# Optimization experiments

Hardware: AMD Instinct MI355X
Metric: run time of the kernel (lower is better)

Reference implementation:

```python
import jax, jax.numpy as jnp
import numpy as np

BN_EPS = 1e-5


def setup_inputs() -> dict:
    key = jax.random.key(0)
    ks = jax.random.split(key, 14)
    B, N, C, NS = 2, 1024, 512, 64
    seed_xyz = jax.random.uniform(ks[0], (B, N, 3), jnp.float32)          # points in unit cube
    seed_features = jax.random.normal(ks[1], (B, C, N), jnp.float32)
    # per-seed rotation matrices (orthonormalized via QR)
    rot = jnp.linalg.qr(jax.random.normal(ks[2], (B, N, 3, 3), jnp.float32))[0]
    # cuboid extents sized so each query finds a reasonable neighbor count
    crop_size = 0.2 + 0.3 * jax.random.uniform(ks[3], (B, N, 3), jnp.float32)
    W1 = jax.random.normal(ks[4], (256, 3 + C), jnp.float32) / np.float32(np.sqrt(3 + C))
    gamma1 = 1.0 + 0.1 * jax.random.normal(ks[5], (256,), jnp.float32)
    beta1 = 0.1 * jax.random.normal(ks[6], (256,), jnp.float32)
    mean1 = 0.1 * jax.random.normal(ks[7], (256,), jnp.float32)
    var1 = 0.5 + jax.random.uniform(ks[8], (256,), jnp.float32)
    W2 = jax.random.normal(ks[9], (256, 256), jnp.float32) / np.float32(16.0)
    gamma2 = 1.0 + 0.1 * jax.random.normal(ks[10], (256,), jnp.float32)
    beta2 = 0.1 * jax.random.normal(ks[11], (256,), jnp.float32)
    mean2 = 0.1 * jax.random.normal(ks[12], (256,), jnp.float32)
    var2 = 0.5 + jax.random.uniform(ks[13], (256,), jnp.float32)
    return dict(seed_xyz=seed_xyz, seed_features=seed_features, rot=rot,
                crop_size=crop_size, W1=W1, gamma1=gamma1, beta1=beta1,
                mean1=mean1, var1=var1, W2=W2, gamma2=gamma2, beta2=beta2,
                mean2=mean2, var2=var2, nsample=NS)


def _conv_bn_relu(x, W, g, b, m, v):
    # 1x1 conv (no bias, bn=True) + inference BatchNorm + ReLU
    y = jnp.einsum('bpnc,oc->bpno', x, W)
    scale = g * jax.lax.rsqrt(v + BN_EPS)
    return jax.nn.relu((y - m) * scale + b)


def reference(seed_xyz, seed_features, rot, crop_size,
              W1, gamma1, beta1, mean1, var1,
              W2, gamma2, beta2, mean2, var2, nsample):
    # ---- rotated rectangular query + group (queries == points == seed_xyz) ----
    # diff[b,p,n] = xyz[b,n] - query[b,p]; rotate into the query's local frame
    diff = seed_xyz[:, None, :, :] - seed_xyz[:, :, None, :]          # (B,P,N,3)
    local = jnp.einsum('bpnj,bpjk->bpnk', diff, rot)                  # (B,P,N,3)
    inside = jnp.all(jnp.abs(local) <= 0.5 * crop_size[:, :, None, :], axis=-1)  # (B,P,N)
    # first `nsample` in-region indices, invalid slots filled with the first hit
    order = jnp.argsort(jnp.where(inside, 0, 1).astype(jnp.int32), axis=-1, stable=True)
    idx = order[..., :nsample]                                        # (B,P,NS)
    valid = jnp.take_along_axis(inside, idx, axis=-1)
    idx = jnp.where(valid, idx, idx[..., :1])
    # gather rotated local xyz and features
    g_xyz = jnp.take_along_axis(local, idx[..., None], axis=2)        # (B,P,NS,3)
    feats = jnp.swapaxes(seed_features, 1, 2)                         # (B,N,C)
    g_feat = jax.vmap(lambda f, i: f[i])(feats, idx)                  # (B,P,NS,C)
    grouped = jnp.concatenate([g_xyz, g_feat], axis=-1)               # (B,P,NS,3+C)
    # ---- SharedMLP (1x1 conv + BN + ReLU) x2, then max over samples ----
    h = _conv_bn_relu(grouped, W1, gamma1, beta1, mean1, var1)
    h = _conv_bn_relu(h, W2, gamma2, beta2, mean2, var2)
    out = jnp.max(h, axis=2)                                          # (B,P,256)
    return jnp.swapaxes(out, 1, 2)                                    # (B,256,P)
```

## Files before the change

kernel.cpp:

```cpp
#include <hip/hip_runtime.h>
#include <hip/hip_bf16.h>
#include <math.h>

typedef __attribute__((ext_vector_type(8))) __bf16 bf16x8;
typedef __attribute__((ext_vector_type(4))) __bf16 bf16x4;
typedef __attribute__((ext_vector_type(2))) __bf16 bf16x2;
typedef __attribute__((ext_vector_type(4))) float f32x4;

#define NPTS 1024
#define CIN 512
#define NSAMP 64
#define LDFT 520
#define LDFO 136

__device__ __forceinline__ void local_coords(const float* q, float cx, float cy, float cz,
                                             const float R[9], float& l0, float& l1, float& l2) {
    float d0 = __fsub_rn(q[0], cx);
    float d1 = __fsub_rn(q[1], cy);
    float d2 = __fsub_rn(q[2], cz);
    l0 = __fadd_rn(__fadd_rn(__fmul_rn(d0, R[0]), __fmul_rn(d1, R[3])), __fmul_rn(d2, R[6]));
    l1 = __fadd_rn(__fadd_rn(__fmul_rn(d0, R[1]), __fmul_rn(d1, R[4])), __fmul_rn(d2, R[7]));
    l2 = __fadd_rn(__fadd_rn(__fmul_rn(d0, R[2]), __fmul_rn(d1, R[5])), __fmul_rn(d2, R[8]));
}

__global__ __launch_bounds__(256) void setup_kernel(
    const float* __restrict__ xyz, const float* __restrict__ rot,
    const float* __restrict__ crop,
    const float* __restrict__ W1, const float* __restrict__ W2,
    const float* __restrict__ g1, const float* __restrict__ be1,
    const float* __restrict__ m1, const float* __restrict__ v1,
    const float* __restrict__ g2, const float* __restrict__ be2,
    const float* __restrict__ m2, const float* __restrict__ v2,
    __bf16* __restrict__ W1f, __bf16* __restrict__ W2s,
    float* __restrict__ wxs,
    float* __restrict__ s1, float* __restrict__ b1,
    float* __restrict__ s2, float* __restrict__ b2,
    unsigned short* __restrict__ seln_g, int* __restrict__ cnt_g,
    f32x4* __restrict__ lcsel_g) {
    __shared__ __align__(16) f32x4 lcall[NPTS];
    __shared__ unsigned long long msk[16];
    __shared__ int wpre[17];
    __shared__ int selr[NSAMP];

    const int t = threadIdx.x;
    if (blockIdx.x < 256) {
        const int o = blockIdx.x;
        if (t == 0) {
            float sc1 = g1[o] / sqrtf(v1[o] + 1e-5f);
            s1[o] = sc1;
            b1[o] = be1[o] - m1[o] * sc1;
            float sc2 = g2[o] / sqrtf(v2[o] + 1e-5f);
            s2[o] = sc2;
            b2[o] = be2[o] - m2[o] * sc2;
            wxs[o * 4 + 0] = sc1 * W1[o * 515 + 0];
            wxs[o * 4 + 1] = sc1 * W1[o * 515 + 1];
            wxs[o * 4 + 2] = sc1 * W1[o * 515 + 2];
            wxs[o * 4 + 3] = 0.f;
        }
        for (int k = t; k < CIN; k += blockDim.x)
            W1f[o * CIN + k] = (__bf16)W1[o * 515 + 3 + k];
        {
            const int f = o * 256 + t;
            const int j = f & 7;
            const int l = (f >> 3) & 63;
            const int nt = (f >> 9) & 1;
            const int ks = (f >> 10) & 7;
            const int w = (f >> 13) & 7;
            const int o2 = w * 32 + nt * 16 + (l & 15);
            const int k = ks * 32 + ((l >> 4) << 3) + j;
            W2s[f] = (__bf16)W2[o2 * 256 + k];
        }
        return;
    }
    const int bid = blockIdx.x - 256;
    const int b = bid >> 10;
    const int l = t & 63, w = t >> 6;

    const float cx = xyz[bid * 3 + 0], cy = xyz[bid * 3 + 1], cz = xyz[bid * 3 + 2];
    float R[9];
#pragma unroll
    for (int j = 0; j < 9; ++j) R[j] = rot[bid * 9 + j];
    const float h0 = 0.5f * crop[bid * 3 + 0];
    const float h1 = 0.5f * crop[bid * 3 + 1];
    const float h2 = 0.5f * crop[bid * 3 + 2];

#pragma unroll
    for (int i = 0; i < 4; ++i) {
        const int n = i * 256 + t;
        float l0, l1, l2;
        local_coords(xyz + (size_t)(b * NPTS + n) * 3, cx, cy, cz, R, l0, l1, l2);
        lcall[n] = f32x4{l0, l1, l2, 0.f};
        bool ins = (__builtin_fabsf(l0) <= h0) && (__builtin_fabsf(l1) <= h1) &&
                   (__builtin_fabsf(l2) <= h2);
        unsigned long long bal = __ballot(ins);
        if (l == 0) msk[i * 4 + w] = bal;
    }
    __syncthreads();
    if (t < 64) {
        const int c = (t < 16) ? __popcll(msk[t]) : 0;
        int sum = c;
#pragma unroll
        for (int d = 1; d < 16; d <<= 1) {
            int v = __shfl_up(sum, d);
            if (t >= d) sum += v;
        }
        if (t < 16) wpre[t] = sum - c;
        if (t == 15) wpre[16] = sum;
    }
    __syncthreads();
    const int cnt = wpre[16];
#pragma unroll
    for (int i = 0; i < 4; ++i) {
        const int n = i * 256 + t;
        const unsigned long long wd = msk[n >> 6];
        const int bit = n & 63;
        if ((wd >> bit) & 1ull) {
            int rank = wpre[n >> 6] + __popcll(wd & ((1ull << bit) - 1ull));
            if (rank < NSAMP) selr[rank] = n;
        }
    }
    __syncthreads();
    if (t < NSAMP) {
        const int n = selr[(t < cnt) ? t : 0];
        seln_g[(size_t)bid * NSAMP + t] = (unsigned short)n;
        lcsel_g[(size_t)bid * NSAMP + t] = lcall[n];
    }
    if (t == 0) cnt_g[bid] = cnt;
}

__global__ __launch_bounds__(256) void fgemm_kernel(const float* __restrict__ feats,
                                                    const __bf16* __restrict__ W1f,
                                                    const float* __restrict__ s1,
                                                    const float* __restrict__ b1,
                                                    __bf16* __restrict__ Fsb) {
    __shared__ __align__(16) __bf16 Ft[16][LDFT];
    __shared__ __align__(16) __bf16 Fo[16][LDFO];
    const int t = threadIdx.x;
    const int b = blockIdx.x >> 7;
    const int half = (blockIdx.x >> 6) & 1;
    const int n0 = (blockIdx.x & 63) << 4;
    const int l = t & 63, w = t >> 6;
    const int lo = l & 15, kg = l >> 4;

    const float* fb = feats + (size_t)b * (CIN * NPTS) + n0;
    {
        const int n = t & 15;
        const int cq = (t >> 4) * 2;
        for (int i = 0; i < 16; ++i) {
            int c = i * 32 + cq;
            float v0 = fb[(size_t)c * NPTS + n];
            float v1v = fb[(size_t)(c + 1) * NPTS + n];
            bf16x2 pk = {(__bf16)v0, (__bf16)v1v};
            *(bf16x2*)(&Ft[n][c]) = pk;
        }
    }
    __syncthreads();

    f32x4 acc[2];
#pragma unroll
    for (int mt = 0; mt < 2; ++mt) acc[mt] = f32x4{0.f, 0.f, 0.f, 0.f};

#pragma unroll
    for (int ks = 0; ks < 16; ++ks) {
        const int kk = ks * 32 + kg * 8;
        const bf16x8 bfr = *(const bf16x8*)(&Ft[lo][kk]);
#pragma unroll
        for (int mt = 0; mt < 2; ++mt) {
            const int o = half * 128 + w * 32 + mt * 16 + lo;
            const bf16x8 af = *(const bf16x8*)(&W1f[(size_t)o * CIN + kk]);
            acc[mt] = __builtin_amdgcn_mfma_f32_16x16x32_bf16(af, bfr, acc[mt], 0, 0, 0);
        }
    }
    __syncthreads();
#pragma unroll
    for (int mt = 0; mt < 2; ++mt) {
        const int ol = w * 32 + mt * 16 + kg * 4;
        const f32x4 sv = *(const f32x4*)(&s1[half * 128 + ol]);
        const f32x4 bv = *(const f32x4*)(&b1[half * 128 + ol]);
        bf16x4 r;
#pragma unroll
        for (int j = 0; j < 4; ++j) r[j] = (__bf16)fmaf(acc[mt][j], sv[j], bv[j]);
        *(bf16x4*)(&Fo[lo][ol]) = r;
    }
    __syncthreads();
    {
        const int row = t >> 4, c = t & 15;
        const bf16x8 v = *(const bf16x8*)(&Fo[row][c * 8]);
        *(bf16x8*)(&Fsb[((size_t)(b * NPTS + n0 + row)) * 256 + half * 128 + c * 8]) = v;
    }
}

__global__ __launch_bounds__(512, 2) void fused_kernel(
    const __bf16* __restrict__ Fsb, const float* __restrict__ wxs,
    const unsigned short* __restrict__ seln_g, const int* __restrict__ cnt_g,
    const f32x4* __restrict__ lcsel_g,
    const __bf16* __restrict__ W2s, const float* __restrict__ s2g, const float* __restrict__ b2g,
    float* __restrict__ out) {
    __shared__ __align__(16) char A2raw[NSAMP * 512];
    __shared__ __align__(16) f32x4 lcL[4][NSAMP];
    __shared__ __align__(16) float outst[256][4];
    __shared__ unsigned short selL[4][NSAMP];
    __shared__ int cntL[4];

    const int raw = (int)blockIdx.x;
    const int pg = (raw & 7) * 64 + (raw >> 3);
    const int b = pg >> 8;
    const int p0 = (pg & 255) * 4;
    const int t = threadIdx.x;
    const int l = t & 63, w = t >> 6;
    const int lo = l & 15, kg = l >> 4;

    if (t < 256) {
        const int pi = t >> 6, s = t & 63;
        const size_t base = ((size_t)(b * NPTS + p0 + pi)) * NSAMP + s;
        selL[pi][s] = seln_g[base];
        lcL[pi][s] = lcsel_g[base];
    }
    if (t >= 256 && t < 260) cntL[t - 256] = cnt_g[b * NPTS + p0 + (t - 256)];

    bf16x8 wf[8][2];
#pragma unroll
    for (int ks = 0; ks < 8; ++ks)
#pragma unroll
        for (int nt = 0; nt < 2; ++nt)
            wf[ks][nt] = *(const bf16x8*)(&W2s[(size_t)((((w * 8 + ks) * 2 + nt) * 64) + l) * 8]);

    const int oc = (t & 31) * 8;
    const int sg = t >> 5;
    f32x4 wv[8];
#pragma unroll
    for (int j = 0; j < 8; ++j) wv[j] = *(const f32x4*)(&wxs[(oc + j) * 4]);

    float sc[2], bb[2];
#pragma unroll
    for (int nt = 0; nt < 2; ++nt) {
        const int o = w * 32 + nt * 16 + lo;
        sc[nt] = s2g[o];
        bb[nt] = b2g[o];
    }
    __syncthreads();

    bf16x8 stg[4];
    {
        const int rpad = (min(cntL[0], NSAMP) + 15) & ~15;
#pragma unroll
        for (int si = 0; si < 4; ++si) {
            const int s = sg * 4 + si;
            if (s < rpad) {
                const int n = (int)selL[0][s];
                stg[si] = *(const bf16x8*)(&Fsb[((size_t)(b * NPTS + n)) * 256 + oc]);
            }
        }
#pragma unroll
        for (int si = 0; si < 4; ++si) {
            const int s = sg * 4 + si;
            if (s < rpad) {
                const f32x4 cd = lcL[0][s];
                bf16x8 pk;
#pragma unroll
                for (int j = 0; j < 8; ++j) {
                    const float x = fmaf(cd.x, wv[j].x,
                                         fmaf(cd.y, wv[j].y,
                                              fmaf(cd.z, wv[j].z, (float)stg[si][j])));
                    pk[j] = (__bf16)fmaxf(x, 0.f);
                }
                *(bf16x8*)(A2raw + s * 512 + ((oc * 2) ^ ((s & 7) << 4))) = pk;
            }
        }
    }
    __syncthreads();

    for (int pi = 0; pi < 4; ++pi) {
        const int mtmax = (min(cntL[pi], NSAMP) + 15) >> 4;

        int rpadn = 0;
        if (pi < 3) {
            rpadn = (min(cntL[pi + 1], NSAMP) + 15) & ~15;
#pragma unroll
            for (int si = 0; si < 4; ++si) {
                const int s = sg * 4 + si;
                if (s < rpadn) {
                    const int n = (int)selL[pi + 1][s];
                    stg[si] = *(const bf16x8*)(&Fsb[((size_t)(b * NPTS + n)) * 256 + oc]);
                }
            }
        }

        f32x4 acc[4][2];
#pragma unroll
        for (int mt = 0; mt < 4; ++mt)
#pragma unroll
            for (int nt = 0; nt < 2; ++nt)
                acc[mt][nt] = f32x4{0.f, 0.f, 0.f, 0.f};

#pragma unroll
        for (int mt = 0; mt < 4; ++mt) {
            if (mt < mtmax) {
                const int row = mt * 16 + lo;
#pragma unroll
                for (int ks = 0; ks < 8; ++ks) {
                    const bf16x8 a = *(const bf16x8*)(A2raw + row * 512 +
                                                      ((ks * 64 + kg * 16) ^ ((row & 7) << 4)));
                    acc[mt][0] = __builtin_amdgcn_mfma_f32_16x16x32_bf16(a, wf[ks][0],
                                                                         acc[mt][0], 0, 0, 0);
                    acc[mt][1] = __builtin_amdgcn_mfma_f32_16x16x32_bf16(a, wf[ks][1],
                                                                         acc[mt][1], 0, 0, 0);
                }
            }
        }

#pragma unroll
        for (int nt = 0; nt < 2; ++nt) {
            float mx = 0.f;
#pragma unroll
            for (int mt = 0; mt < 4; ++mt) {
                if (mt < mtmax) {
#pragma unroll
                    for (int r = 0; r < 4; ++r)
                        mx = fmaxf(mx, fmaxf(fmaf(acc[mt][nt][r], sc[nt], bb[nt]), 0.f));
                }
            }
            mx = fmaxf(mx, __shfl_xor(mx, 16));
            mx = fmaxf(mx, __shfl_xor(mx, 32));
            if (kg == 0) outst[w * 32 + nt * 16 + lo][pi] = mx;
        }
        __syncthreads();

        if (pi < 3) {
#pragma unroll
            for (int si = 0; si < 4; ++si) {
                const int s = sg * 4 + si;
                if (s < rpadn) {
                    const f32x4 cd = lcL[pi + 1][s];
                    bf16x8 pk;
#pragma unroll
                    for (int j = 0; j < 8; ++j) {
                        const float x = fmaf(cd.x, wv[j].x,
                                             fmaf(cd.y, wv[j].y,
                                                  fmaf(cd.z, wv[j].z, (float)stg[si][j])));
                        pk[j] = (__bf16)fmaxf(x, 0.f);
                    }
                    *(bf16x8*)(A2raw + s * 512 + ((oc * 2) ^ ((s & 7) << 4))) = pk;
                }
            }
        }
        __syncthreads();
    }

    if (t < 256) {
        const int o = t;
        const f32x4 v = *(const f32x4*)(&outst[o][0]);
        *(f32x4*)(&out[((size_t)b * 256 + o) * NPTS + p0]) = v;
    }
}

extern "C" void kernel_launch(void* const* d_in, const int* in_sizes, int n_in,
                              void* d_out, int out_size, void* d_ws, size_t ws_size,
                              hipStream_t stream) {
    (void)in_sizes; (void)n_in; (void)out_size; (void)ws_size;
    const float* xyz   = (const float*)d_in[0];
    const float* feats = (const float*)d_in[1];
    const float* rot   = (const float*)d_in[2];
    const float* crop  = (const float*)d_in[3];
    const float* W1    = (const float*)d_in[4];
    const float* g1    = (const float*)d_in[5];
    const float* be1   = (const float*)d_in[6];
    const float* m1    = (const float*)d_in[7];
    const float* v1    = (const float*)d_in[8];
    const float* W2    = (const float*)d_in[9];
    const float* g2    = (const float*)d_in[10];
    const float* be2   = (const float*)d_in[11];
    const float* m2    = (const float*)d_in[12];
    const float* v2    = (const float*)d_in[13];

    char* ws = (char*)d_ws;
    __bf16* W1f = (__bf16*)(ws + 0);
    __bf16* W2s = (__bf16*)(ws + 262144);
    float*  wxs = (float*)(ws + 393216);
    float*  s1  = (float*)(ws + 397312);
    float*  b1  = (float*)(ws + 398336);
    float*  s2  = (float*)(ws + 399360);
    float*  b2  = (float*)(ws + 400384);
    __bf16* Fsb = (__bf16*)(ws + 401408);
    unsigned short* seln = (unsigned short*)(ws + 1449984);
    int*    cntg = (int*)(ws + 1712128);
    f32x4*  lcse = (f32x4*)(ws + 1720320);

    setup_kernel<<<2304, 256, 0, stream>>>(xyz, rot, crop,
                                           W1, W2, g1, be1, m1, v1, g2, be2, m2, v2,
                                           W1f, W2s, wxs, s1, b1, s2, b2, seln, cntg, lcse);
    fgemm_kernel<<<256, 256, 0, stream>>>(feats, W1f, s1, b1, Fsb);
    fused_kernel<<<512, 512, 0, stream>>>(Fsb, wxs, seln, cntg, lcse, W2s, s2, b2,
                                          (float*)d_out);
}
```

Baseline: 46.53 us.

## Merge feature GEMM into setup kernel and restructure fused-kernel gather staging

Folds the feature×W1 GEMM into the setup kernel as extra blocks. It reads W1 fp32 directly with an inline bf16 conversion instead of going through a pre-converted W1f buffer, which removes one kernel launch and its dependency on setup. The fused kernel now gives each thread 4 channels × 8 samples instead of 8 × 4, moves the xyz-term FMA and ReLU to before the max-reduction barrier, and raises launch_bounds occupancy from 2 to 4. Costs: W1 is reread and converted per block, and register pressure is tighter at the higher occupancy.

```diff
diff --git a/kernel.cpp b/kernel.cpp
--- a/kernel.cpp
+++ b/kernel.cpp
@@ -25,30 +25,92 @@
 
 __global__ __launch_bounds__(256) void setup_kernel(
     const float* __restrict__ xyz, const float* __restrict__ rot,
-    const float* __restrict__ crop,
+    const float* __restrict__ crop, const float* __restrict__ feats,
     const float* __restrict__ W1, const float* __restrict__ W2,
     const float* __restrict__ g1, const float* __restrict__ be1,
     const float* __restrict__ m1, const float* __restrict__ v1,
     const float* __restrict__ g2, const float* __restrict__ be2,
     const float* __restrict__ m2, const float* __restrict__ v2,
-    __bf16* __restrict__ W1f, __bf16* __restrict__ W2s,
-    float* __restrict__ wxs,
-    float* __restrict__ s1, float* __restrict__ b1,
+    __bf16* __restrict__ W2s, float* __restrict__ wxs,
     float* __restrict__ s2, float* __restrict__ b2,
+    __bf16* __restrict__ Fsb,
     unsigned short* __restrict__ seln_g, int* __restrict__ cnt_g,
     f32x4* __restrict__ lcsel_g) {
-    __shared__ __align__(16) f32x4 lcall[NPTS];
-    __shared__ unsigned long long msk[16];
-    __shared__ int wpre[17];
-    __shared__ int selr[NSAMP];
-
+    __shared__ __align__(16) char U[22016];
     const int t = threadIdx.x;
+
     if (blockIdx.x < 256) {
-        const int o = blockIdx.x;
+        __bf16(*Ft)[LDFT] = (__bf16(*)[LDFT])(U);
+        __bf16(*Fo)[LDFO] = (__bf16(*)[LDFO])(U + 16640);
+        float* s1l = (float*)(U + 20992);
+        float* b1l = (float*)(U + 21504);
+        const int rb = blockIdx.x;
+        const int b = rb >> 7, half = (rb >> 6) & 1, n0 = (rb & 63) << 4;
+        const int l = t & 63, w = t >> 6;
+        const int lo = l & 15, kg = l >> 4;
+
+        if (t < 128) {
+            const int o = half * 128 + t;
+            const float s = g1[o] / sqrtf(v1[o] + 1e-5f);
+            s1l[t] = s;
+            b1l[t] = be1[o] - m1[o] * s;
+        }
+        const float* fb = feats + (size_t)b * (CIN * NPTS) + n0;
+        {
+            const int n = t & 15;
+            const int cq = (t >> 4) * 2;
+            for (int i = 0; i < 16; ++i) {
+                int c = i * 32 + cq;
+                float v0 = fb[(size_t)c * NPTS + n];
+                float v1v = fb[(size_t)(c + 1) * NPTS + n];
+                bf16x2 pk = {(__bf16)v0, (__bf16)v1v};
+                *(bf16x2*)(&Ft[n][c]) = pk;
+            }
+        }
+        __syncthreads();
+
+        f32x4 acc[2];
+#pragma unroll
+        for (int mt = 0; mt < 2; ++mt) acc[mt] = f32x4{0.f, 0.f, 0.f, 0.f};
+
+#pragma unroll
+        for (int ks = 0; ks < 16; ++ks) {
+            const int kk = ks * 32 + kg * 8;
+            const bf16x8 bfr = *(const bf16x8*)(&Ft[lo][kk]);
+#pragma unroll
+            for (int mt = 0; mt < 2; ++mt) {
+                const int o = half * 128 + w * 32 + mt * 16 + lo;
+                const float* wrow = W1 + (size_t)o * 515 + 3 + kk;
+                bf16x8 af;
+#pragma unroll
+                for (int j = 0; j < 8; ++j) af[j] = (__bf16)wrow[j];
+                acc[mt] = __builtin_amdgcn_mfma_f32_16x16x32_bf16(af, bfr, acc[mt], 0, 0, 0);
+            }
+        }
+        __syncthreads();
+#pragma unroll
+        for (int mt = 0; mt < 2; ++mt) {
+            const int ol = w * 32 + mt * 16 + kg * 4;
+            const f32x4 sv = *(const f32x4*)(&s1l[ol]);
+            const f32x4 bv = *(const f32x4*)(&b1l[ol]);
+            bf16x4 r;
+#pragma unroll
+            for (int j = 0; j < 4; ++j) r[j] = (__bf16)fmaf(acc[mt][j], sv[j], bv[j]);
+            *(bf16x4*)(&Fo[lo][ol]) = r;
+        }
+        __syncthreads();
+        {
+            const int row = t >> 4, c = t & 15;
+            const bf16x8 v = *(const bf16x8*)(&Fo[row][c * 8]);
+            *(bf16x8*)(&Fsb[((size_t)(b * NPTS + n0 + row)) * 256 + half * 128 + c * 8]) = v;
+        }
+        return;
+    }
+
+    if (blockIdx.x < 512) {
+        const int o = blockIdx.x - 256;
         if (t == 0) {
             float sc1 = g1[o] / sqrtf(v1[o] + 1e-5f);
-            s1[o] = sc1;
-            b1[o] = be1[o] - m1[o] * sc1;
             float sc2 = g2[o] / sqrtf(v2[o] + 1e-5f);
             s2[o] = sc2;
             b2[o] = be2[o] - m2[o] * sc2;
@@ -57,8 +119,6 @@
             wxs[o * 4 + 2] = sc1 * W1[o * 515 + 2];
             wxs[o * 4 + 3] = 0.f;
         }
-        for (int k = t; k < CIN; k += blockDim.x)
-            W1f[o * CIN + k] = (__bf16)W1[o * 515 + 3 + k];
         {
             const int f = o * 256 + t;
             const int j = f & 7;
@@ -72,7 +132,12 @@
         }
         return;
     }
-    const int bid = blockIdx.x - 256;
+
+    f32x4* lcall = (f32x4*)(U);
+    unsigned long long* msk = (unsigned long long*)(U + 16384);
+    int* wpre = (int*)(U + 16512);
+    int* selr = (int*)(U + 16584);
+    const int bid = blockIdx.x - 512;
     const int b = bid >> 10;
     const int l = t & 63, w = t >> 6;
 
@@ -128,69 +193,7 @@
     if (t == 0) cnt_g[bid] = cnt;
 }
 
-__global__ __launch_bounds__(256) void fgemm_kernel(const float* __restrict__ feats,
-                                                    const __bf16* __restrict__ W1f,
-                                                    const float* __restrict__ s1,
-                                                    const float* __restrict__ b1,
-                                                    __bf16* __restrict__ Fsb) {
-    __shared__ __align__(16) __bf16 Ft[16][LDFT];
-    __shared__ __align__(16) __bf16 Fo[16][LDFO];
-    const int t = threadIdx.x;
-    const int b = blockIdx.x >> 7;
-    const int half = (blockIdx.x >> 6) & 1;
-    const int n0 = (blockIdx.x & 63) << 4;
-    const int l = t & 63, w = t >> 6;
-    const int lo = l & 15, kg = l >> 4;
-
-    const float* fb = feats + (size_t)b * (CIN * NPTS) + n0;
-    {
-        const int n = t & 15;
-        const int cq = (t >> 4) * 2;
-        for (int i = 0; i < 16; ++i) {
-            int c = i * 32 + cq;
-            float v0 = fb[(size_t)c * NPTS + n];
-            float v1v = fb[(size_t)(c + 1) * NPTS + n];
-            bf16x2 pk = {(__bf16)v0, (__bf16)v1v};
-            *(bf16x2*)(&Ft[n][c]) = pk;
-        }
-    }
-    __syncthreads();
-
-    f32x4 acc[2];
-#pragma unroll
-    for (int mt = 0; mt < 2; ++mt) acc[mt] = f32x4{0.f, 0.f, 0.f, 0.f};
-
-#pragma unroll
-    for (int ks = 0; ks < 16; ++ks) {
-        const int kk = ks * 32 + kg * 8;
-        const bf16x8 bfr = *(const bf16x8*)(&Ft[lo][kk]);
-#pragma unroll
-        for (int mt = 0; mt < 2; ++mt) {
-            const int o = half * 128 + w * 32 + mt * 16 + lo;
-            const bf16x8 af = *(const bf16x8*)(&W1f[(size_t)o * CIN + kk]);
-            acc[mt] = __builtin_amdgcn_mfma_f32_16x16x32_bf16(af, bfr, acc[mt], 0, 0, 0);
-        }
-    }
-    __syncthreads();
-#pragma unroll
-    for (int mt = 0; mt < 2; ++mt) {
-        const int ol = w * 32 + mt * 16 + kg * 4;
-        const f32x4 sv = *(const f32x4*)(&s1[half * 128 + ol]);
-        const f32x4 bv = *(const f32x4*)(&b1[half * 128 + ol]);
-        bf16x4 r;
-#pragma unroll
-        for (int j = 0; j < 4; ++j) r[j] = (__bf16)fmaf(acc[mt][j], sv[j], bv[j]);
-        *(bf16x4*)(&Fo[lo][ol]) = r;
-    }
-    __syncthreads();
-    {
-        const int row = t >> 4, c = t & 15;
-        const bf16x8 v = *(const bf16x8*)(&Fo[row][c * 8]);
-        *(bf16x8*)(&Fsb[((size_t)(b * NPTS + n0 + row)) * 256 + half * 128 + c * 8]) = v;
-    }
-}
-
-__global__ __launch_bounds__(512, 2) void fused_kernel(
+__global__ __launch_bounds__(512, 4) void fused_kernel(
     const __bf16* __restrict__ Fsb, const float* __restrict__ wxs,
     const unsigned short* __restrict__ seln_g, const int* __restrict__ cnt_g,
     const f32x4* __restrict__ lcsel_g,
@@ -225,11 +228,11 @@
         for (int nt = 0; nt < 2; ++nt)
             wf[ks][nt] = *(const bf16x8*)(&W2s[(size_t)((((w * 8 + ks) * 2 + nt) * 64) + l) * 8]);
 
-    const int oc = (t & 31) * 8;
-    const int sg = t >> 5;
-    f32x4 wv[8];
-#pragma unroll
-    for (int j = 0; j < 8; ++j) wv[j] = *(const f32x4*)(&wxs[(oc + j) * 4]);
+    const int oc4 = (t & 63) * 4;
+    const int g8 = t >> 6;
+    f32x4 wv4[4];
+#pragma unroll
+    for (int j = 0; j < 4; ++j) wv4[j] = *(const f32x4*)(&wxs[(oc4 + j) * 4]);
 
     float sc[2], bb[2];
 #pragma unroll
@@ -240,31 +243,30 @@
     }
     __syncthreads();
 
-    bf16x8 stg[4];
+    bf16x4 stg[8];
     {
         const int rpad = (min(cntL[0], NSAMP) + 15) & ~15;
 #pragma unroll
-        for (int si = 0; si < 4; ++si) {
-            const int s = sg * 4 + si;
+        for (int si = 0; si < 8; ++si) {
+            const int s = g8 * 8 + si;
             if (s < rpad) {
                 const int n = (int)selL[0][s];
-                stg[si] = *(const bf16x8*)(&Fsb[((size_t)(b * NPTS + n)) * 256 + oc]);
-            }
-        }
-#pragma unroll
-        for (int si = 0; si < 4; ++si) {
-            const int s = sg * 4 + si;
+                stg[si] = *(const bf16x4*)(&Fsb[((size_t)(b * NPTS + n)) * 256 + oc4]);
+            }
+        }
+#pragma unroll
+        for (int si = 0; si < 8; ++si) {
+            const int s = g8 * 8 + si;
             if (s < rpad) {
                 const f32x4 cd = lcL[0][s];
-                bf16x8 pk;
-#pragma unroll
-                for (int j = 0; j < 8; ++j) {
-                    const float x = fmaf(cd.x, wv[j].x,
-                                         fmaf(cd.y, wv[j].y,
-                                              fmaf(cd.z, wv[j].z, (float)stg[si][j])));
-                    pk[j] = (__bf16)fmaxf(x, 0.f);
-                }
-                *(bf16x8*)(A2raw + s * 512 + ((oc * 2) ^ ((s & 7) << 4))) = pk;
+#pragma unroll
+                for (int j = 0; j < 4; ++j) {
+                    const float x = fmaf(cd.x, wv4[j].x,
+                                         fmaf(cd.y, wv4[j].y,
+                                              fmaf(cd.z, wv4[j].z, (float)stg[si][j])));
+                    stg[si][j] = (__bf16)fmaxf(x, 0.f);
+                }
+                *(bf16x4*)(A2raw + s * 512 + ((oc4 * 2) ^ ((s & 7) << 4))) = stg[si];
             }
         }
     }
@@ -272,16 +274,15 @@
 
     for (int pi = 0; pi < 4; ++pi) {
         const int mtmax = (min(cntL[pi], NSAMP) + 15) >> 4;
-
         int rpadn = 0;
         if (pi < 3) {
             rpadn = (min(cntL[pi + 1], NSAMP) + 15) & ~15;
 #pragma unroll
-            for (int si = 0; si < 4; ++si) {
-                const int s = sg * 4 + si;
+            for (int si = 0; si < 8; ++si) {
+                const int s = g8 * 8 + si;
                 if (s < rpadn) {
                     const int n = (int)selL[pi + 1][s];
-                    stg[si] = *(const bf16x8*)(&Fsb[((size_t)(b * NPTS + n)) * 256 + oc]);
+                    stg[si] = *(const bf16x4*)(&Fsb[((size_t)(b * NPTS + n)) * 256 + oc4]);
                 }
             }
         }
@@ -309,6 +310,23 @@
             }
         }
 
+        if (pi < 3) {
+#pragma unroll
+            for (int si = 0; si < 8; ++si) {
+                const int s = g8 * 8 + si;
+                if (s < rpadn) {
+                    const f32x4 cd = lcL[pi + 1][s];
+#pragma unroll
+                    for (int j = 0; j < 4; ++j) {
+                        const float x = fmaf(cd.x, wv4[j].x,
+                                             fmaf(cd.y, wv4[j].y,
+                                                  fmaf(cd.z, wv4[j].z, (float)stg[si][j])));
+                        stg[si][j] = (__bf16)fmaxf(x, 0.f);
+                    }
+                }
+            }
+        }
+
 #pragma unroll
         for (int nt = 0; nt < 2; ++nt) {
             float mx = 0.f;
@@ -328,20 +346,10 @@
 
         if (pi < 3) {
 #pragma unroll
-            for (int si = 0; si < 4; ++si) {
-                const int s = sg * 4 + si;
-                if (s < rpadn) {
-                    const f32x4 cd = lcL[pi + 1][s];
-                    bf16x8 pk;
-#pragma unroll
-                    for (int j = 0; j < 8; ++j) {
-                        const float x = fmaf(cd.x, wv[j].x,
-                                             fmaf(cd.y, wv[j].y,
-                                                  fmaf(cd.z, wv[j].z, (float)stg[si][j])));
-                        pk[j] = (__bf16)fmaxf(x, 0.f);
-                    }
-                    *(bf16x8*)(A2raw + s * 512 + ((oc * 2) ^ ((s & 7) << 4))) = pk;
-                }
+            for (int si = 0; si < 8; ++si) {
+                const int s = g8 * 8 + si;
+                if (s < rpadn)
+                    *(bf16x4*)(A2raw + s * 512 + ((oc4 * 2) ^ ((s & 7) << 4))) = stg[si];
             }
         }
         __syncthreads();
@@ -374,22 +382,18 @@
     const float* v2    = (const float*)d_in[13];
 
     char* ws = (char*)d_ws;
-    __bf16* W1f = (__bf16*)(ws + 0);
-    __bf16* W2s = (__bf16*)(ws + 262144);
-    float*  wxs = (float*)(ws + 393216);
-    float*  s1  = (float*)(ws + 397312);
-    float*  b1  = (float*)(ws + 398336);
-    float*  s2  = (float*)(ws + 399360);
-    float*  b2  = (float*)(ws + 400384);
-    __bf16* Fsb = (__bf16*)(ws + 401408);
-    unsigned short* seln = (unsigned short*)(ws + 1449984);
-    int*    cntg = (int*)(ws + 1712128);
-    f32x4*  lcse = (f32x4*)(ws + 1720320);
-
-    setup_kernel<<<2304, 256, 0, stream>>>(xyz, rot, crop,
+    __bf16* W2s = (__bf16*)(ws + 0);
+    float*  wxs = (float*)(ws + 131072);
+    float*  s2  = (float*)(ws + 135168);
+    float*  b2  = (float*)(ws + 136192);
+    __bf16* Fsb = (__bf16*)(ws + 137216);
+    unsigned short* seln = (unsigned short*)(ws + 1185792);
+    int*    cntg = (int*)(ws + 1447936);
+    f32x4*  lcse = (f32x4*)(ws + 1456128);
+
+    setup_kernel<<<2560, 256, 0, stream>>>(xyz, rot, crop, feats,
                                            W1, W2, g1, be1, m1, v1, g2, be2, m2, v2,
-                                           W1f, W2s, wxs, s1, b1, s2, b2, seln, cntg, lcse);
-    fgemm_kernel<<<256, 256, 0, stream>>>(feats, W1f, s1, b1, Fsb);
+                                           W2s, wxs, s2, b2, Fsb, seln, cntg, lcse);
     fused_kernel<<<512, 512, 0, stream>>>(Fsb, wxs, seln, cntg, lcse, W2s, s2, b2,
                                           (float*)d_out);
 }
```

After: 110.7 us. 2.38x slower.

## Process eight query points per block and overlap layer-1 epilogue with MFMA

Applied to the files above, without the earlier changes.

Each fused-kernel block now handles eight query points instead of four, so half as many blocks are launched and the W2 register fragments are loaded once per eight points. The gather split changes from eight channels per thread to four channels over eight samples. The per-sample xyz correction and ReLU for the next point is now computed in registers right after the MFMA loop and before the barrier, leaving only the shared-memory store after it. In exchange, 256 blocks fill fewer CUs and each block runs a longer serial chain.

```diff
diff --git a/kernel.cpp b/kernel.cpp
--- a/kernel.cpp
+++ b/kernel.cpp
@@ -197,26 +197,26 @@
     const __bf16* __restrict__ W2s, const float* __restrict__ s2g, const float* __restrict__ b2g,
     float* __restrict__ out) {
     __shared__ __align__(16) char A2raw[NSAMP * 512];
-    __shared__ __align__(16) f32x4 lcL[4][NSAMP];
-    __shared__ __align__(16) float outst[256][4];
-    __shared__ unsigned short selL[4][NSAMP];
-    __shared__ int cntL[4];
+    __shared__ __align__(16) f32x4 lcL[8][NSAMP];
+    __shared__ __align__(16) float outst[256][8];
+    __shared__ unsigned short selL[8][NSAMP];
+    __shared__ int cntL[8];
 
     const int raw = (int)blockIdx.x;
-    const int pg = (raw & 7) * 64 + (raw >> 3);
-    const int b = pg >> 8;
-    const int p0 = (pg & 255) * 4;
+    const int pg = (raw & 7) * 32 + (raw >> 3);
+    const int b = pg >> 7;
+    const int p0 = (pg & 127) * 8;
     const int t = threadIdx.x;
     const int l = t & 63, w = t >> 6;
     const int lo = l & 15, kg = l >> 4;
 
-    if (t < 256) {
+    {
         const int pi = t >> 6, s = t & 63;
         const size_t base = ((size_t)(b * NPTS + p0 + pi)) * NSAMP + s;
         selL[pi][s] = seln_g[base];
         lcL[pi][s] = lcsel_g[base];
     }
-    if (t >= 256 && t < 260) cntL[t - 256] = cnt_g[b * NPTS + p0 + (t - 256)];
+    if (t < 8) cntL[t] = cnt_g[b * NPTS + p0 + t];
 
     bf16x8 wf[8][2];
 #pragma unroll
@@ -225,11 +225,11 @@
         for (int nt = 0; nt < 2; ++nt)
             wf[ks][nt] = *(const bf16x8*)(&W2s[(size_t)((((w * 8 + ks) * 2 + nt) * 64) + l) * 8]);
 
-    const int oc = (t & 31) * 8;
-    const int sg = t >> 5;
-    f32x4 wv[8];
-#pragma unroll
-    for (int j = 0; j < 8; ++j) wv[j] = *(const f32x4*)(&wxs[(oc + j) * 4]);
+    const int oc4 = (t & 63) * 4;
+    const int g8 = t >> 6;
+    f32x4 wv4[4];
+#pragma unroll
+    for (int j = 0; j < 4; ++j) wv4[j] = *(const f32x4*)(&wxs[(oc4 + j) * 4]);
 
     float sc[2], bb[2];
 #pragma unroll
@@ -240,48 +240,46 @@
     }
     __syncthreads();
 
-    bf16x8 stg[4];
+    bf16x4 stg[8];
     {
         const int rpad = (min(cntL[0], NSAMP) + 15) & ~15;
 #pragma unroll
-        for (int si = 0; si < 4; ++si) {
-            const int s = sg * 4 + si;
+        for (int si = 0; si < 8; ++si) {
+            const int s = g8 * 8 + si;
             if (s < rpad) {
                 const int n = (int)selL[0][s];
-                stg[si] = *(const bf16x8*)(&Fsb[((size_t)(b * NPTS + n)) * 256 + oc]);
-            }
-        }
-#pragma unroll
-        for (int si = 0; si < 4; ++si) {
-            const int s = sg * 4 + si;
+                stg[si] = *(const bf16x4*)(&Fsb[((size_t)(b * NPTS + n)) * 256 + oc4]);
+            }
+        }
+#pragma unroll
+        for (int si = 0; si < 8; ++si) {
+            const int s = g8 * 8 + si;
             if (s < rpad) {
                 const f32x4 cd = lcL[0][s];
-                bf16x8 pk;
-#pragma unroll
-                for (int j = 0; j < 8; ++j) {
-                    const float x = fmaf(cd.x, wv[j].x,
-                                         fmaf(cd.y, wv[j].y,
-                                              fmaf(cd.z, wv[j].z, (float)stg[si][j])));
-                    pk[j] = (__bf16)fmaxf(x, 0.f);
+#pragma unroll
+                for (int j = 0; j < 4; ++j) {
+                    const float x = fmaf(cd.x, wv4[j].x,
+                                         fmaf(cd.y, wv4[j].y,
+                                              fmaf(cd.z, wv4[j].z, (float)stg[si][j])));
+                    stg[si][j] = (__bf16)fmaxf(x, 0.f);
                 }
-                *(bf16x8*)(A2raw + s * 512 + ((oc * 2) ^ ((s & 7) << 4))) = pk;
-            }
-        }
-    }
-    __syncthreads();
-
-    for (int pi = 0; pi < 4; ++pi) {
+                *(bf16x4*)(A2raw + s * 512 + ((oc4 * 2) ^ ((s & 7) << 4))) = stg[si];
+            }
+        }
+    }
+    __syncthreads();
+
+    for (int pi = 0; pi < 8; ++pi) {
         const int mtmax = (min(cntL[pi], NSAMP) + 15) >> 4;
-
         int rpadn = 0;
-        if (pi < 3) {
+        if (pi < 7) {
             rpadn = (min(cntL[pi + 1], NSAMP) + 15) & ~15;
 #pragma unroll
-            for (int si = 0; si < 4; ++si) {
-                const int s = sg * 4 + si;
+            for (int si = 0; si < 8; ++si) {
+                const int s = g8 * 8 + si;
                 if (s < rpadn) {
                     const int n = (int)selL[pi + 1][s];
-                    stg[si] = *(const bf16x8*)(&Fsb[((size_t)(b * NPTS + n)) * 256 + oc]);
+                    stg[si] = *(const bf16x4*)(&Fsb[((size_t)(b * NPTS + n)) * 256 + oc4]);
                 }
             }
         }
@@ -309,6 +307,23 @@
             }
         }
 
+        if (pi < 7) {
+#pragma unroll
+            for (int si = 0; si < 8; ++si) {
+                const int s = g8 * 8 + si;
+                if (s < rpadn) {
+                    const f32x4 cd = lcL[pi + 1][s];
+#pragma unroll
+                    for (int j = 0; j < 4; ++j) {
+                        const float x = fmaf(cd.x, wv4[j].x,
+                                             fmaf(cd.y, wv4[j].y,
+                                                  fmaf(cd.z, wv4[j].z, (float)stg[si][j])));
+                        stg[si][j] = (__bf16)fmaxf(x, 0.f);
+                    }
+                }
+            }
+        }
+
 #pragma unroll
         for (int nt = 0; nt < 2; ++nt) {
             float mx = 0.f;
@@ -326,31 +341,21 @@
         }
         __syncthreads();
 
-        if (pi < 3) {
-#pragma unroll
-            for (int si = 0; si < 4; ++si) {
-                const int s = sg * 4 + si;
-                if (s < rpadn) {
-                    const f32x4 cd = lcL[pi + 1][s];
-                    bf16x8 pk;
-#pragma unroll
-                    for (int j = 0; j < 8; ++j) {
-                        const float x = fmaf(cd.x, wv[j].x,
-                                             fmaf(cd.y, wv[j].y,
-                                                  fmaf(cd.z, wv[j].z, (float)stg[si][j])));
-                        pk[j] = (__bf16)fmaxf(x, 0.f);
-                    }
-                    *(bf16x8*)(A2raw + s * 512 + ((oc * 2) ^ ((s & 7) << 4))) = pk;
-                }
+        if (pi < 7) {
+#pragma unroll
+            for (int si = 0; si < 8; ++si) {
+                const int s = g8 * 8 + si;
+                if (s < rpadn)
+                    *(bf16x4*)(A2raw + s * 512 + ((oc4 * 2) ^ ((s & 7) << 4))) = stg[si];
             }
         }
         __syncthreads();
     }
 
-    if (t < 256) {
-        const int o = t;
-        const f32x4 v = *(const f32x4*)(&outst[o][0]);
-        *(f32x4*)(&out[((size_t)b * 256 + o) * NPTS + p0]) = v;
+    {
+        const int o = t >> 1, hf = t & 1;
+        const f32x4 v = *(const f32x4*)(&outst[o][hf * 4]);
+        *(f32x4*)(&out[((size_t)b * 256 + o) * NPTS + p0 + hf * 4]) = v;
     }
 }
 
@@ -390,6 +395,6 @@
                                            W1, W2, g1, be1, m1, v1, g2, be2, m2, v2,
                                            W1f, W2s, wxs, s1, b1, s2, b2, seln, cntg, lcse);
     fgemm_kernel<<<256, 256, 0, stream>>>(feats, W1f, s1, b1, Fsb);
-    fused_kernel<<<512, 512, 0, stream>>>(Fsb, wxs, seln, cntg, lcse, W2s, s2, b2,
+    fused_kernel<<<256, 512, 0, stream>>>(Fsb, wxs, seln, cntg, lcse, W2s, s2, b2,
                                           (float*)d_out);
 }
```

New measurement: 44.16 us. 1.05x faster.

## Switch to fp16 with packed xyz transform and double-buffered grouping in fused kernel

Applied to the files above, without the earlier changes.

Moves all intermediate tensors and MFMA operands from bf16 to fp16. The xyz-term and ReLU in the gather transform now use packed half2 math instead of fp32 FMAs. The fused kernel double-buffers the A2 tile in LDS, which removes one barrier per point, drops the staging of selections in shared memory, and raises the occupancy hint to 4. fp16 changes range and precision and could overflow or diverge from the reference, and the double buffer doubles LDS use.

```diff
diff --git a/kernel.cpp b/kernel.cpp
--- a/kernel.cpp
+++ b/kernel.cpp
@@ -2,10 +2,12 @@
 #include <hip/hip_bf16.h>
 #include <math.h>
 
-typedef __attribute__((ext_vector_type(8))) __bf16 bf16x8;
-typedef __attribute__((ext_vector_type(4))) __bf16 bf16x4;
-typedef __attribute__((ext_vector_type(2))) __bf16 bf16x2;
+typedef __attribute__((ext_vector_type(8))) _Float16 f16x8;
+typedef __attribute__((ext_vector_type(4))) _Float16 f16x4;
+typedef __attribute__((ext_vector_type(2))) _Float16 f16x2;
 typedef __attribute__((ext_vector_type(4))) float f32x4;
+typedef __attribute__((ext_vector_type(8))) unsigned short u16x8;
+typedef __attribute__((ext_vector_type(4))) int i32x4;
 
 #define NPTS 1024
 #define CIN 512
@@ -31,12 +33,12 @@
     const float* __restrict__ m1, const float* __restrict__ v1,
     const float* __restrict__ g2, const float* __restrict__ be2,
     const float* __restrict__ m2, const float* __restrict__ v2,
-    __bf16* __restrict__ W1f, __bf16* __restrict__ W2s,
-    float* __restrict__ wxs,
+    _Float16* __restrict__ W1h, _Float16* __restrict__ W2s,
+    _Float16* __restrict__ wxh,
     float* __restrict__ s1, float* __restrict__ b1,
     float* __restrict__ s2, float* __restrict__ b2,
     unsigned short* __restrict__ seln_g, int* __restrict__ cnt_g,
-    f32x4* __restrict__ lcsel_g) {
+    _Float16* __restrict__ lch_g) {
     __shared__ __align__(16) f32x4 lcall[NPTS];
     __shared__ unsigned long long msk[16];
     __shared__ int wpre[17];
@@ -52,13 +54,9 @@
             float sc2 = g2[o] / sqrtf(v2[o] + 1e-5f);
             s2[o] = sc2;
             b2[o] = be2[o] - m2[o] * sc2;
-            wxs[o * 4 + 0] = sc1 * W1[o * 515 + 0];
-            wxs[o * 4 + 1] = sc1 * W1[o * 515 + 1];
-            wxs[o * 4 + 2] = sc1 * W1[o * 515 + 2];
-            wxs[o * 4 + 3] = 0.f;
         }
         for (int k = t; k < CIN; k += blockDim.x)
-            W1f[o * CIN + k] = (__bf16)W1[o * 515 + 3 + k];
+            W1h[o * CIN + k] = (_Float16)W1[o * 515 + 3 + k];
         {
             const int f = o * 256 + t;
             const int j = f & 7;
@@ -68,7 +66,17 @@
             const int w = (f >> 13) & 7;
             const int o2 = w * 32 + nt * 16 + (l & 15);
             const int k = ks * 32 + ((l >> 4) << 3) + j;
-            W2s[f] = (__bf16)W2[o2 * 256 + k];
+            W2s[f] = (_Float16)W2[o2 * 256 + k];
+        }
+        if (o == 0 && t < 192) {
+            const int g = t / 3, c = t % 3;
+#pragma unroll
+            for (int ph = 0; ph < 4; ++ph) {
+                const int oo = g * 4 + ph;
+                const float sc1 = g1[oo] / sqrtf(v1[oo] + 1e-5f);
+                const float val = sc1 * W1[(size_t)oo * 515 + c];
+                wxh[g * 16 + ((ph >= 2) ? 8 : 0) + c * 2 + (ph & 1)] = (_Float16)val;
+            }
         }
         return;
     }
@@ -123,18 +131,21 @@
     if (t < NSAMP) {
         const int n = selr[(t < cnt) ? t : 0];
         seln_g[(size_t)bid * NSAMP + t] = (unsigned short)n;
-        lcsel_g[(size_t)bid * NSAMP + t] = lcall[n];
+        const f32x4 c4 = lcall[n];
+        const _Float16 h0h = (_Float16)c4.x, h1h = (_Float16)c4.y, h2h = (_Float16)c4.z;
+        f16x8 pk = {h0h, h0h, h1h, h1h, h2h, h2h, (_Float16)0, (_Float16)0};
+        *(f16x8*)(lch_g + ((size_t)bid * NSAMP + t) * 8) = pk;
     }
     if (t == 0) cnt_g[bid] = cnt;
 }
 
 __global__ __launch_bounds__(256) void fgemm_kernel(const float* __restrict__ feats,
-                                                    const __bf16* __restrict__ W1f,
+                                                    const _Float16* __restrict__ W1h,
                                                     const float* __restrict__ s1,
                                                     const float* __restrict__ b1,
-                                                    __bf16* __restrict__ Fsb) {
-    __shared__ __align__(16) __bf16 Ft[16][LDFT];
-    __shared__ __align__(16) __bf16 Fo[16][LDFO];
+                                                    _Float16* __restrict__ Fsh) {
+    __shared__ __align__(16) _Float16 Ft[16][LDFT];
+    __shared__ __align__(16) _Float16 Fo[16][LDFO];
     const int t = threadIdx.x;
     const int b = blockIdx.x >> 7;
     const int half = (blockIdx.x >> 6) & 1;
@@ -150,8 +161,8 @@
             int c = i * 32 + cq;
             float v0 = fb[(size_t)c * NPTS + n];
             float v1v = fb[(size_t)(c + 1) * NPTS + n];
-            bf16x2 pk = {(__bf16)v0, (__bf16)v1v};
-            *(bf16x2*)(&Ft[n][c]) = pk;
+            f16x2 pk = {(_Float16)v0, (_Float16)v1v};
+            *(f16x2*)(&Ft[n][c]) = pk;
         }
     }
     __syncthreads();
@@ -163,12 +174,12 @@
 #pragma unroll
     for (int ks = 0; ks < 16; ++ks) {
         const int kk = ks * 32 + kg * 8;
-        const bf16x8 bfr = *(const bf16x8*)(&Ft[lo][kk]);
+        const f16x8 bfr = *(const f16x8*)(&Ft[lo][kk]);
 #pragma unroll
         for (int mt = 0; mt < 2; ++mt) {
             const int o = half * 128 + w * 32 + mt * 16 + lo;
-            const bf16x8 af = *(const bf16x8*)(&W1f[(size_t)o * CIN + kk]);
-            acc[mt] = __builtin_amdgcn_mfma_f32_16x16x32_bf16(af, bfr, acc[mt], 0, 0, 0);
+            const f16x8 af = *(const f16x8*)(&W1h[(size_t)o * CIN + kk]);
+            acc[mt] = __builtin_amdgcn_mfma_f32_16x16x32_f16(af, bfr, acc[mt], 0, 0, 0);
         }
     }
     __syncthreads();
@@ -177,30 +188,27 @@
         const int ol = w * 32 + mt * 16 + kg * 4;
         const f32x4 sv = *(const f32x4*)(&s1[half * 128 + ol]);
         const f32x4 bv = *(const f32x4*)(&b1[half * 128 + ol]);
-        bf16x4 r;
-#pragma unroll
-        for (int j = 0; j < 4; ++j) r[j] = (__bf16)fmaf(acc[mt][j], sv[j], bv[j]);
-        *(bf16x4*)(&Fo[lo][ol]) = r;
+        f16x4 r;
+#pragma unroll
+        for (int j = 0; j < 4; ++j) r[j] = (_Float16)fmaf(acc[mt][j], sv[j], bv[j]);
+        *(f16x4*)(&Fo[lo][ol]) = r;
     }
     __syncthreads();
     {
         const int row = t >> 4, c = t & 15;
-        const bf16x8 v = *(const bf16x8*)(&Fo[row][c * 8]);
-        *(bf16x8*)(&Fsb[((size_t)(b * NPTS + n0 + row)) * 256 + half * 128 + c * 8]) = v;
-    }
-}
-
-__global__ __launch_bounds__(512, 2) void fused_kernel(
-    const __bf16* __restrict__ Fsb, const float* __restrict__ wxs,
+        const f16x8 v = *(const f16x8*)(&Fo[row][c * 8]);
+        *(f16x8*)(&Fsh[((size_t)(b * NPTS + n0 + row)) * 256 + half * 128 + c * 8]) = v;
+    }
+}
+
+__global__ __launch_bounds__(512, 4) void fused_kernel(
+    const _Float16* __restrict__ Fsh, const _Float16* __restrict__ wxh,
     const unsigned short* __restrict__ seln_g, const int* __restrict__ cnt_g,
-    const f32x4* __restrict__ lcsel_g,
-    const __bf16* __restrict__ W2s, const float* __restrict__ s2g, const float* __restrict__ b2g,
+    const _Float16* __restrict__ lch_g,
+    const _Float16* __restrict__ W2s, const float* __restrict__ s2g, const float* __restrict__ b2g,
     float* __restrict__ out) {
-    __shared__ __align__(16) char A2raw[NSAMP * 512];
-    __shared__ __align__(16) f32x4 lcL[4][NSAMP];
+    __shared__ __align__(16) char A2raw[2][NSAMP * 512];
     __shared__ __align__(16) float outst[256][4];
-    __shared__ unsigned short selL[4][NSAMP];
-    __shared__ int cntL[4];
 
     const int raw = (int)blockIdx.x;
     const int pg = (raw & 7) * 64 + (raw >> 3);
@@ -209,27 +217,33 @@
     const int t = threadIdx.x;
     const int l = t & 63, w = t >> 6;
     const int lo = l & 15, kg = l >> 4;
-
-    if (t < 256) {
-        const int pi = t >> 6, s = t & 63;
-        const size_t base = ((size_t)(b * NPTS + p0 + pi)) * NSAMP + s;
-        selL[pi][s] = seln_g[base];
-        lcL[pi][s] = lcsel_g[base];
-    }
-    if (t >= 256 && t < 260) cntL[t - 256] = cnt_g[b * NPTS + p0 + (t - 256)];
-
-    bf16x8 wf[8][2];
+    const int oc4 = (t & 63) * 4;
+    const int g8 = t >> 6;
+
+    f16x8 wf[8][2];
 #pragma unroll
     for (int ks = 0; ks < 8; ++ks)
 #pragma unroll
         for (int nt = 0; nt < 2; ++nt)
-            wf[ks][nt] = *(const bf16x8*)(&W2s[(size_t)((((w * 8 + ks) * 2 + nt) * 64) + l) * 8]);
-
-    const int oc = (t & 31) * 8;
-    const int sg = t >> 5;
-    f32x4 wv[8];
-#pragma unroll
-    for (int j = 0; j < 8; ++j) wv[j] = *(const f32x4*)(&wxs[(oc + j) * 4]);
+            wf[ks][nt] = *(const f16x8*)(&W2s[(size_t)((((w * 8 + ks) * 2 + nt) * 64) + l) * 8]);
+
+    f16x2 wx0, wy0, wz0, wx1, wy1, wz1;
+    {
+        const int g = t & 63;
+        const f16x8 a = *(const f16x8*)(wxh + g * 16);
+        const f16x8 c = *(const f16x8*)(wxh + g * 16 + 8);
+        wx0 = f16x2{a[0], a[1]}; wy0 = f16x2{a[2], a[3]}; wz0 = f16x2{a[4], a[5]};
+        wx1 = f16x2{c[0], c[1]}; wy1 = f16x2{c[2], c[3]}; wz1 = f16x2{c[4], c[5]};
+    }
+
+    const i32x4 cnt4 = *(const i32x4*)(cnt_g + (b * NPTS + p0));
+    int rp[4], mtm[4];
+#pragma unroll
+    for (int pl = 0; pl < 4; ++pl) {
+        const int rn = min(cnt4[pl], NSAMP);
+        rp[pl] = (rn + 15) & ~15;
+        mtm[pl] = (rn + 15) >> 4;
+    }
 
     float sc[2], bb[2];
 #pragma unroll
@@ -238,54 +252,38 @@
         sc[nt] = s2g[o];
         bb[nt] = b2g[o];
     }
-    __syncthreads();
-
-    bf16x8 stg[4];
-    {
-        const int rpad = (min(cntL[0], NSAMP) + 15) & ~15;
-#pragma unroll
-        for (int si = 0; si < 4; ++si) {
-            const int s = sg * 4 + si;
-            if (s < rpad) {
-                const int n = (int)selL[0][s];
-                stg[si] = *(const bf16x8*)(&Fsb[((size_t)(b * NPTS + n)) * 256 + oc]);
+
+    const f16x2 zz = {};
+
+    auto do_transform = [&](int pl, int dst) {
+        const u16x8 sl = *(const u16x8*)(seln_g + ((size_t)(b * NPTS + p0 + pl)) * NSAMP + g8 * 8);
+        const int rpl = rp[pl];
+#pragma unroll
+        for (int si = 0; si < 8; ++si) {
+            const int s = g8 * 8 + si;
+            if (s < rpl) {
+                const int n = (int)sl[si];
+                const f16x4 f = *(const f16x4*)(Fsh + ((size_t)(b * NPTS + n)) * 256 + oc4);
+                const f16x8 lc = *(const f16x8*)(lch_g + (((size_t)(b * NPTS + p0 + pl)) * NSAMP + s) * 8);
+                const f16x2 lx = {lc[0], lc[1]}, ly = {lc[2], lc[3]}, lz = {lc[4], lc[5]};
+                f16x2 f0 = {f[0], f[1]}, f1 = {f[2], f[3]};
+                f0 = lz * wz0 + f0; f0 = ly * wy0 + f0; f0 = lx * wx0 + f0;
+                f1 = lz * wz1 + f1; f1 = ly * wy1 + f1; f1 = lx * wx1 + f1;
+                f0 = __builtin_elementwise_max(f0, zz);
+                f1 = __builtin_elementwise_max(f1, zz);
+                const f16x4 r = {f0[0], f0[1], f1[0], f1[1]};
+                *(f16x4*)(A2raw[dst] + s * 512 + ((oc4 * 2) ^ ((s & 7) << 4))) = r;
             }
         }
-#pragma unroll
-        for (int si = 0; si < 4; ++si) {
-            const int s = sg * 4 + si;
-            if (s < rpad) {
-                const f32x4 cd = lcL[0][s];
-                bf16x8 pk;
-#pragma unroll
-                for (int j = 0; j < 8; ++j) {
-                    const float x = fmaf(cd.x, wv[j].x,
-                                         fmaf(cd.y, wv[j].y,
-                                              fmaf(cd.z, wv[j].z, (float)stg[si][j])));
-                    pk[j] = (__bf16)fmaxf(x, 0.f);
-                }
-                *(bf16x8*)(A2raw + s * 512 + ((oc * 2) ^ ((s & 7) << 4))) = pk;
-            }
-        }
-    }
+    };
+
+    do_transform(0, 0);
     __syncthreads();
 
     for (int pi = 0; pi < 4; ++pi) {
-        const int mtmax = (min(cntL[pi], NSAMP) + 15) >> 4;
-
-        int rpadn = 0;
-        if (pi < 3) {
-            rpadn = (min(cntL[pi + 1], NSAMP) + 15) & ~15;
-#pragma unroll
-            for (int si = 0; si < 4; ++si) {
-                const int s = sg * 4 + si;
-                if (s < rpadn) {
-                    const int n = (int)selL[pi + 1][s];
-                    stg[si] = *(const bf16x8*)(&Fsb[((size_t)(b * NPTS + n)) * 256 + oc]);
-                }
-            }
-        }
-
+        if (pi < 3) do_transform(pi + 1, (pi + 1) & 1);
+
+        const int mtmax = mtm[pi];
         f32x4 acc[4][2];
 #pragma unroll
         for (int mt = 0; mt < 4; ++mt)
@@ -299,12 +297,12 @@
                 const int row = mt * 16 + lo;
 #pragma unroll
                 for (int ks = 0; ks < 8; ++ks) {
-                    const bf16x8 a = *(const bf16x8*)(A2raw + row * 512 +
-                                                      ((ks * 64 + kg * 16) ^ ((row & 7) << 4)));
-                    acc[mt][0] = __builtin_amdgcn_mfma_f32_16x16x32_bf16(a, wf[ks][0],
-                                                                         acc[mt][0], 0, 0, 0);
-                    acc[mt][1] = __builtin_amdgcn_mfma_f32_16x16x32_bf16(a, wf[ks][1],
-                                                                         acc[mt][1], 0, 0, 0);
+                    const f16x8 a = *(const f16x8*)(A2raw[pi & 1] + row * 512 +
+                                                    ((ks * 64 + kg * 16) ^ ((row & 7) << 4)));
+                    acc[mt][0] = __builtin_amdgcn_mfma_f32_16x16x32_f16(a, wf[ks][0],
+                                                                        acc[mt][0], 0, 0, 0);
+                    acc[mt][1] = __builtin_amdgcn_mfma_f32_16x16x32_f16(a, wf[ks][1],
+                                                                        acc[mt][1], 0, 0, 0);
                 }
             }
         }
@@ -323,26 +321,6 @@
             mx = fmaxf(mx, __shfl_xor(mx, 16));
             mx = fmaxf(mx, __shfl_xor(mx, 32));
             if (kg == 0) outst[w * 32 + nt * 16 + lo][pi] = mx;
-        }
-        __syncthreads();
-
-        if (pi < 3) {
-#pragma unroll
-            for (int si = 0; si < 4; ++si) {
-                const int s = sg * 4 + si;
-                if (s < rpadn) {
-                    const f32x4 cd = lcL[pi + 1][s];
-                    bf16x8 pk;
-#pragma unroll
-                    for (int j = 0; j < 8; ++j) {
-                        const float x = fmaf(cd.x, wv[j].x,
-                                             fmaf(cd.y, wv[j].y,
-                                                  fmaf(cd.z, wv[j].z, (float)stg[si][j])));
-                        pk[j] = (__bf16)fmaxf(x, 0.f);
-                    }
-                    *(bf16x8*)(A2raw + s * 512 + ((oc * 2) ^ ((s & 7) << 4))) = pk;
-                }
-            }
         }
         __syncthreads();
     }
@@ -374,22 +352,22 @@
     const float* v2    = (const float*)d_in[13];
 
     char* ws = (char*)d_ws;
-    __bf16* W1f = (__bf16*)(ws + 0);
-    __bf16* W2s = (__bf16*)(ws + 262144);
-    float*  wxs = (float*)(ws + 393216);
-    float*  s1  = (float*)(ws + 397312);
-    float*  b1  = (float*)(ws + 398336);
-    float*  s2  = (float*)(ws + 399360);
-    float*  b2  = (float*)(ws + 400384);
-    __bf16* Fsb = (__bf16*)(ws + 401408);
-    unsigned short* seln = (unsigned short*)(ws + 1449984);
-    int*    cntg = (int*)(ws + 1712128);
-    f32x4*  lcse = (f32x4*)(ws + 1720320);
+    _Float16* W1h = (_Float16*)(ws + 0);
+    _Float16* W2s = (_Float16*)(ws + 262144);
+    _Float16* wxh = (_Float16*)(ws + 393216);
+    float*  s1  = (float*)(ws + 395264);
+    float*  b1  = (float*)(ws + 396288);
+    float*  s2  = (float*)(ws + 397312);
+    float*  b2  = (float*)(ws + 398336);
+    _Float16* Fsh = (_Float16*)(ws + 399360);
+    unsigned short* seln = (unsigned short*)(ws + 1447936);
+    int*    cntg = (int*)(ws + 1710080);
+    _Float16* lch = (_Float16*)(ws + 1718272);
 
     setup_kernel<<<2304, 256, 0, stream>>>(xyz, rot, crop,
                                            W1, W2, g1, be1, m1, v1, g2, be2, m2, v2,
-                                           W1f, W2s, wxs, s1, b1, s2, b2, seln, cntg, lcse);
-    fgemm_kernel<<<256, 256, 0, stream>>>(feats, W1f, s1, b1, Fsb);
-    fused_kernel<<<512, 512, 0, stream>>>(Fsb, wxs, seln, cntg, lcse, W2s, s2, b2,
+                                           W1h, W2s, wxh, s1, b1, s2, b2, seln, cntg, lch);
+    fgemm_kernel<<<256, 256, 0, stream>>>(feats, W1h, s1, b1, Fsh);
+    fused_kernel<<<512, 512, 0, stream>>>(Fsh, wxh, seln, cntg, lch, W2s, s2, b2,
                                           (float*)d_out);
 }
```

Result: slower. 62.86 us (+35.1%).
